# Kernel optimization log

Hardware: AMD Instinct MI355X
Metric: run time of the kernel (lower is better)

Reference implementation:

```python
import jax, jax.numpy as jnp
import numpy as np

EMB = 1024
HEADS = 16
SCALE = (EMB // HEADS) ** (-0.5)


def setup_inputs() -> dict:
    key = jax.random.key(0)
    k1, k2, k3, k4, k5 = jax.random.split(key, 5)
    x = jax.random.normal(k1, (2, 2048, EMB), dtype=jnp.float32)
    w_qkv = jax.random.normal(k2, (EMB, 3 * EMB), dtype=jnp.float32) * (EMB ** -0.5)
    b_qkv = jax.random.normal(k3, (3 * EMB,), dtype=jnp.float32) * 0.02
    w_proj = jax.random.normal(k4, (EMB, EMB), dtype=jnp.float32) * (EMB ** -0.5)
    b_proj = jax.random.normal(k5, (EMB,), dtype=jnp.float32) * 0.02
    return {"x": x, "w_qkv": w_qkv, "b_qkv": b_qkv, "w_proj": w_proj, "b_proj": b_proj}


def reference(x, w_qkv, b_qkv, w_proj, b_proj):
    b, n, d = x.shape
    # qkv projection; split last dim as (heads, head_dim, 3) exactly like the
    # torch reshape, then permute to (3, b, h, n, head_dim)
    qkv = (x @ w_qkv + b_qkv).reshape(b, n, HEADS, -1, 3)
    qkv = jnp.transpose(qkv, (4, 0, 2, 1, 3))
    q, k, v = qkv[0], qkv[1], qkv[2]
    energy = jnp.einsum('bhqd,bhkd->bhqk', q, k)  # full n x n scores
    att = jax.nn.softmax(energy, axis=-1) * SCALE  # softmax THEN scale (as in source)
    out = jnp.einsum('bhqk,bhkd->bhqd', att, v)
    out = jnp.transpose(out, (0, 2, 1, 3)).reshape(b, n, d)
    return out @ w_proj + b_proj
```

## Files before the change

kernel.cpp:

```cpp
#include <hip/hip_runtime.h>
#include <cstdint>

#define SEQ   2048
#define BATCH 2
#define EMB   1024
#define NH    16
#define HD    64
#define MROWS (BATCH*SEQ)
#define NQKV  (3*EMB)
#define SCALE 0.125f
#define L2E   1.4426950408889634f

typedef _Float16 half8 __attribute__((ext_vector_type(8)));
typedef _Float16 half4 __attribute__((ext_vector_type(4)));
typedef __fp16   fp16x2 __attribute__((ext_vector_type(2)));
typedef float    floatx4 __attribute__((ext_vector_type(4)));

#define MFMA(a,b,c) __builtin_amdgcn_mfma_f32_16x16x32_f16(a, b, c, 0, 0, 0)

__device__ __forceinline__ void async16(const void* g, const void* l) {
    __builtin_amdgcn_global_load_lds(
        (const __attribute__((address_space(1))) unsigned int*)(uintptr_t)g,
        (__attribute__((address_space(3))) unsigned int*)(uint32_t)(uintptr_t)l,
        16, 0, 0);
}

__global__ void k_split(const float* __restrict__ src, _Float16* __restrict__ hi, int n4) {
    int i = blockIdx.x * blockDim.x + threadIdx.x;
    if (i >= n4) return;
    float4 v = ((const float4*)src)[i];
    half4 h;
    h[0] = (_Float16)v.x;
    h[1] = (_Float16)v.y;
    h[2] = (_Float16)v.z;
    h[3] = (_Float16)v.w;
    ((half4*)hi)[i] = h;
}

__global__ void k_transpose_split(const float* __restrict__ w, _Float16* __restrict__ hi,
                                  int K, int N) {
    __shared__ float t[32][33];
    int n0 = blockIdx.x * 32, k0 = blockIdx.y * 32;
    int tx = threadIdx.x, ty = threadIdx.y;
    #pragma unroll
    for (int i = 0; i < 4; i++)
        t[ty + i * 8][tx] = w[(size_t)(k0 + ty + i * 8) * N + n0 + tx];
    __syncthreads();
    #pragma unroll
    for (int i = 0; i < 4; i++) {
        float v = t[tx][ty + i * 8];
        hi[(size_t)(n0 + ty + i * 8) * K + k0 + tx] = (_Float16)v;
    }
}

template<int MODE>
__global__ __launch_bounds__(256, 2)
void k_gemm(const _Float16* __restrict__ A, const _Float16* __restrict__ Bt,
            const float* __restrict__ bias,
            _Float16* __restrict__ outQ, _Float16* __restrict__ outK,
            _Float16* __restrict__ outV, float* __restrict__ outC,
            int Mdim, int Ndim, int Kdim) {
    __shared__ _Float16 smem[2 * 128 * 32];
    _Float16* As = smem;
    _Float16* Bs = smem + 4096;

    const int tid = threadIdx.x;
    const int lane = tid & 63, wid = tid >> 6;
    const int quad = lane >> 4, l16 = lane & 15;
    const int wm = (wid >> 1) * 64, wn = (wid & 1) * 64;
    const int m0 = blockIdx.y * 128, n0 = blockIdx.x * 128;

    floatx4 acc[4][4];
    #pragma unroll
    for (int i = 0; i < 4; i++)
        #pragma unroll
        for (int j = 0; j < 4; j++)
            acc[i][j] = (floatx4){0.f, 0.f, 0.f, 0.f};

    for (int k0 = 0; k0 < Kdim; k0 += 32) {
        __syncthreads();
        #pragma unroll
        for (int i = 0; i < 2; i++) {
            int c = i * 256 + tid;
            int row = c >> 2, slot = c & 3;
            int q = slot ^ ((row >> 1) & 3);
            async16(A  + (size_t)(m0 + row) * Kdim + k0 + q * 8, As + c * 8);
            async16(Bt + (size_t)(n0 + row) * Kdim + k0 + q * 8, Bs + c * 8);
        }
        __syncthreads();

        half8 af[4], bf[4];
        #pragma unroll
        for (int t = 0; t < 4; t++) {
            int rowA = wm + t * 16 + l16;
            af[t] = *(const half8*)(As + rowA * 32 + (quad ^ ((rowA >> 1) & 3)) * 8);
            int rowB = wn + t * 16 + l16;
            bf[t] = *(const half8*)(Bs + rowB * 32 + (quad ^ ((rowB >> 1) & 3)) * 8);
        }
        #pragma unroll
        for (int mt = 0; mt < 4; mt++)
            #pragma unroll
            for (int nt = 0; nt < 4; nt++)
                acc[mt][nt] = MFMA(af[mt], bf[nt], acc[mt][nt]);
    }

    #pragma unroll
    for (int mt = 0; mt < 4; mt++) {
        int rowg = m0 + wm + mt * 16 + quad * 4;
        #pragma unroll
        for (int nt = 0; nt < 4; nt++) {
            int colg = n0 + wn + nt * 16 + l16;
            float bv = bias[colg];
            if (MODE == 0) {
                int h = colg / 192, rem = colg % 192;
                int d = rem / 3, which = rem % 3;
                #pragma unroll
                for (int r = 0; r < 4; r++) {
                    int m = rowg + r;
                    int b = m >> 11, s = m & (SEQ - 1);
                    int bh = b * NH + h;
                    _Float16 hv = (_Float16)(acc[mt][nt][r] + bv);
                    if (which == 0)      outQ[((size_t)bh * SEQ + s) * HD + d] = hv;
                    else if (which == 1) outK[((size_t)bh * SEQ + s) * HD + d] = hv;
                    else                 outV[((size_t)bh * HD + d) * SEQ + s] = hv;
                }
            } else {
                #pragma unroll
                for (int r = 0; r < 4; r++)
                    outC[(size_t)(rowg + r) * Ndim + colg] = acc[mt][nt][r] + bv;
            }
        }
    }
}

__device__ __forceinline__ int swzK(int row) { return (row ^ (row >> 2)) & 7; }
__device__ __forceinline__ int swzV(int row) { return (row ^ (row >> 1)) & 7; }

__global__ __launch_bounds__(256, 2)
void k_attn(const _Float16* __restrict__ Q, const _Float16* __restrict__ K,
            const _Float16* __restrict__ Vt, _Float16* __restrict__ Aout) {
    __shared__ __align__(16) _Float16 Ks[128 * 64];
    __shared__ __align__(16) _Float16 Vs[64 * 128];

    const int tid = threadIdx.x;
    const int lane = tid & 63, wid = tid >> 6;
    const int quad = lane >> 4, l16 = lane & 15;

    const int n = blockIdx.x;
    const int bh = (n & 7) * 4 + (n >> 7);
    const int q0 = ((n >> 3) & 15) * 128;

    const _Float16* Qb = Q  + (size_t)bh * SEQ * HD;
    const _Float16* Kb = K  + (size_t)bh * SEQ * HD;
    const _Float16* Vb = Vt + (size_t)bh * HD * SEQ;

    const int rA = ((l16 >> 2) << 3) | (l16 & 3);
    const int grayl = (l16 ^ (l16 >> 1)) & 7;

    half8 qf[2][2];
    #pragma unroll
    for (int qt = 0; qt < 2; qt++)
        #pragma unroll
        for (int kc = 0; kc < 2; kc++)
            qf[qt][kc] = *(const half8*)(Qb + (size_t)(q0 + wid * 32 + qt * 16 + l16) * HD
                                          + kc * 32 + quad * 8);

    floatx4 o[2][4];
    float mi[2] = {-1e30f, -1e30f}, li[2] = {0.f, 0.f};
    #pragma unroll
    for (int qt = 0; qt < 2; qt++)
        #pragma unroll
        for (int dt = 0; dt < 4; dt++) o[qt][dt] = (floatx4){0.f, 0.f, 0.f, 0.f};

    for (int kv0 = 0; kv0 < SEQ; kv0 += 128) {
        __syncthreads();
        #pragma unroll
        for (int i = 0; i < 4; i++) {
            int c = i * 256 + tid;
            {
                int row = c >> 3, pos = c & 7;
                int q = pos ^ swzK(row);
                async16(Kb + (size_t)(kv0 + row) * HD + q * 8, Ks + c * 8);
            }
            {
                int row = c >> 4, pos = c & 15;
                int q = (pos & 8) | ((pos & 7) ^ swzV(row));
                async16(Vb + (size_t)row * SEQ + kv0 + q * 8, Vs + c * 8);
            }
        }
        __syncthreads();

        floatx4 sv[4][2][2];
        #pragma unroll
        for (int u = 0; u < 4; u++)
            #pragma unroll
            for (int e = 0; e < 2; e++) {
                int row = u * 32 + e * 4 + rA;
                int sw = swzK(row);
                const _Float16* base = Ks + row * 64;
                half8 kf0 = *(const half8*)(base + ((quad ^ sw) << 3));
                half8 kf1 = *(const half8*)(base + (((quad + 4) ^ sw) << 3));
                floatx4 z = (floatx4){0.f, 0.f, 0.f, 0.f};
                #pragma unroll
                for (int qt = 0; qt < 2; qt++) {
                    floatx4 s = MFMA(kf0, qf[qt][0], z);
                    sv[u][e][qt] = MFMA(kf1, qf[qt][1], s);
                }
            }

        #pragma unroll
        for (int qt = 0; qt < 2; qt++) {
            float mb = -1e30f;
            #pragma unroll
            for (int u = 0; u < 4; u++)
                #pragma unroll
                for (int e = 0; e < 2; e++)
                    #pragma unroll
                    for (int r = 0; r < 4; r++)
                        mb = fmaxf(mb, sv[u][e][qt][r]);
            mb = fmaxf(mb, __shfl_xor(mb, 16));
            mb = fmaxf(mb, __shfl_xor(mb, 32));
            float Mn = fmaxf(mi[qt], mb * L2E);
            float al = __builtin_amdgcn_exp2f(mi[qt] - Mn);
            mi[qt] = Mn;
            li[qt] *= al;
            float alq[4];
            #pragma unroll
            for (int r = 0; r < 4; r++)
                alq[r] = __shfl(al, quad * 4 + r);
            #pragma unroll
            for (int dt = 0; dt < 4; dt++)
                #pragma unroll
                for (int r = 0; r < 4; r++)
                    o[qt][dt][r] *= alq[r];
        }

        #pragma unroll
        for (int u = 0; u < 4; u++) {
            half8 af[2];
            #pragma unroll
            for (int qt = 0; qt < 2; qt++) {
                float p[8];
                float rs = 0.f;
                #pragma unroll
                for (int r = 0; r < 4; r++) {
                    p[r]     = __builtin_amdgcn_exp2f(fmaf(sv[u][0][qt][r], L2E, -mi[qt]));
                    p[4 + r] = __builtin_amdgcn_exp2f(fmaf(sv[u][1][qt][r], L2E, -mi[qt]));
                }
                #pragma unroll
                for (int r = 0; r < 8; r++) rs += p[r];
                li[qt] += rs;
                union { fp16x2 h2[4]; half8 v; } pk;
                pk.h2[0] = __builtin_amdgcn_cvt_pkrtz(p[0], p[1]);
                pk.h2[1] = __builtin_amdgcn_cvt_pkrtz(p[2], p[3]);
                pk.h2[2] = __builtin_amdgcn_cvt_pkrtz(p[4], p[5]);
                pk.h2[3] = __builtin_amdgcn_cvt_pkrtz(p[6], p[7]);
                af[qt] = pk.v;
            }
            int q = u * 4 + quad;
            int slotbase = (q & 8) | ((q & 7) ^ grayl);
            #pragma unroll
            for (int dt = 0; dt < 4; dt++) {
                int row = dt * 16 + l16;
                half8 vf = *(const half8*)(Vs + row * 128 + slotbase * 8);
                o[0][dt] = MFMA(af[0], vf, o[0][dt]);
                o[1][dt] = MFMA(af[1], vf, o[1][dt]);
            }
        }
    }

    float lv[2];
    #pragma unroll
    for (int qt = 0; qt < 2; qt++) {
        float l = li[qt];
        l += __shfl_xor(l, 16);
        l += __shfl_xor(l, 32);
        lv[qt] = l;
    }
    int b = bh >> 4, h = bh & 15;
    #pragma unroll
    for (int qt = 0; qt < 2; qt++)
        #pragma unroll
        for (int r = 0; r < 4; r++) {
            float l = __shfl(lv[qt], quad * 4 + r);
            float inv = SCALE / l;
            int srow = q0 + wid * 32 + qt * 16 + quad * 4 + r;
            #pragma unroll
            for (int dt = 0; dt < 4; dt++) {
                int col = h * HD + dt * 16 + l16;
                Aout[(size_t)(b * SEQ + srow) * EMB + col] = (_Float16)(o[qt][dt][r] * inv);
            }
        }
}

extern "C" void kernel_launch(void* const* d_in, const int* in_sizes, int n_in,
                              void* d_out, int out_size, void* d_ws, size_t ws_size,
                              hipStream_t stream) {
    (void)in_sizes; (void)n_in; (void)out_size; (void)ws_size;
    const float* x      = (const float*)d_in[0];
    const float* w_qkv  = (const float*)d_in[1];
    const float* b_qkv  = (const float*)d_in[2];
    const float* w_proj = (const float*)d_in[3];
    const float* b_proj = (const float*)d_in[4];

    char* ws = (char*)d_ws;
    const size_t MB = 1ull << 20;
    _Float16* x_hi  = (_Float16*)(ws + 0 * MB);
    _Float16* wq_hi = (_Float16*)(ws + 8 * MB);
    _Float16* wp_hi = (_Float16*)(ws + 14 * MB);
    _Float16* Qb    = (_Float16*)(ws + 16 * MB);
    _Float16* Kb    = (_Float16*)(ws + 24 * MB);
    _Float16* Vtb   = (_Float16*)(ws + 32 * MB);
    _Float16* attb  = (_Float16*)(ws + 40 * MB);

    k_split<<<(MROWS * EMB / 4) / 256, 256, 0, stream>>>(x, x_hi, MROWS * EMB / 4);
    k_transpose_split<<<dim3(NQKV / 32, EMB / 32), dim3(32, 8), 0, stream>>>(
        w_qkv, wq_hi, EMB, NQKV);
    k_transpose_split<<<dim3(EMB / 32, EMB / 32), dim3(32, 8), 0, stream>>>(
        w_proj, wp_hi, EMB, EMB);
    k_gemm<0><<<dim3(NQKV / 128, MROWS / 128), 256, 0, stream>>>(
        x_hi, wq_hi, b_qkv, Qb, Kb, Vtb, nullptr, MROWS, NQKV, EMB);
    k_attn<<<dim3(512), 256, 0, stream>>>(Qb, Kb, Vtb, attb);
    k_gemm<1><<<dim3(EMB / 128, MROWS / 128), 256, 0, stream>>>(
        attb, wp_hi, b_proj, nullptr, nullptr, nullptr,
        (float*)d_out, MROWS, EMB, EMB);
}
```

Baseline: 209.8 us.

## Double-buffer attention K/V loads, compute row sums via MFMA, narrow proj GEMM tile

```diff
diff --git a/kernel.cpp b/kernel.cpp
--- a/kernel.cpp
+++ b/kernel.cpp
@@ -53,28 +53,30 @@
     }
 }
 
-template<int MODE>
+template<int MODE, int NT>
 __global__ __launch_bounds__(256, 2)
 void k_gemm(const _Float16* __restrict__ A, const _Float16* __restrict__ Bt,
             const float* __restrict__ bias,
             _Float16* __restrict__ outQ, _Float16* __restrict__ outK,
             _Float16* __restrict__ outV, float* __restrict__ outC,
             int Mdim, int Ndim, int Kdim) {
-    __shared__ _Float16 smem[2 * 128 * 32];
+    constexpr int WN  = NT / 2;
+    constexpr int NTI = WN / 16;
+    __shared__ _Float16 smem[(128 + NT) * 32];
     _Float16* As = smem;
-    _Float16* Bs = smem + 4096;
+    _Float16* Bs = smem + 128 * 32;
 
     const int tid = threadIdx.x;
     const int lane = tid & 63, wid = tid >> 6;
     const int quad = lane >> 4, l16 = lane & 15;
-    const int wm = (wid >> 1) * 64, wn = (wid & 1) * 64;
-    const int m0 = blockIdx.y * 128, n0 = blockIdx.x * 128;
-
-    floatx4 acc[4][4];
+    const int wm = (wid >> 1) * 64, wn = (wid & 1) * WN;
+    const int m0 = blockIdx.y * 128, n0 = blockIdx.x * NT;
+
+    floatx4 acc[4][NTI];
     #pragma unroll
     for (int i = 0; i < 4; i++)
         #pragma unroll
-        for (int j = 0; j < 4; j++)
+        for (int j = 0; j < NTI; j++)
             acc[i][j] = (floatx4){0.f, 0.f, 0.f, 0.f};
 
     for (int k0 = 0; k0 < Kdim; k0 += 32) {
@@ -84,23 +86,32 @@
             int c = i * 256 + tid;
             int row = c >> 2, slot = c & 3;
             int q = slot ^ ((row >> 1) & 3);
-            async16(A  + (size_t)(m0 + row) * Kdim + k0 + q * 8, As + c * 8);
+            async16(A + (size_t)(m0 + row) * Kdim + k0 + q * 8, As + c * 8);
+        }
+        #pragma unroll
+        for (int i = 0; i < NT / 64; i++) {
+            int c = i * 256 + tid;
+            int row = c >> 2, slot = c & 3;
+            int q = slot ^ ((row >> 1) & 3);
             async16(Bt + (size_t)(n0 + row) * Kdim + k0 + q * 8, Bs + c * 8);
         }
         __syncthreads();
 
-        half8 af[4], bf[4];
+        half8 af[4], bf[NTI];
         #pragma unroll
         for (int t = 0; t < 4; t++) {
             int rowA = wm + t * 16 + l16;
             af[t] = *(const half8*)(As + rowA * 32 + (quad ^ ((rowA >> 1) & 3)) * 8);
+        }
+        #pragma unroll
+        for (int t = 0; t < NTI; t++) {
             int rowB = wn + t * 16 + l16;
             bf[t] = *(const half8*)(Bs + rowB * 32 + (quad ^ ((rowB >> 1) & 3)) * 8);
         }
         #pragma unroll
         for (int mt = 0; mt < 4; mt++)
             #pragma unroll
-            for (int nt = 0; nt < 4; nt++)
+            for (int nt = 0; nt < NTI; nt++)
                 acc[mt][nt] = MFMA(af[mt], bf[nt], acc[mt][nt]);
     }
 
@@ -108,7 +119,7 @@
     for (int mt = 0; mt < 4; mt++) {
         int rowg = m0 + wm + mt * 16 + quad * 4;
         #pragma unroll
-        for (int nt = 0; nt < 4; nt++) {
+        for (int nt = 0; nt < NTI; nt++) {
             int colg = n0 + wn + nt * 16 + l16;
             float bv = bias[colg];
             if (MODE == 0) {
@@ -139,8 +150,8 @@
 __global__ __launch_bounds__(256, 2)
 void k_attn(const _Float16* __restrict__ Q, const _Float16* __restrict__ K,
             const _Float16* __restrict__ Vt, _Float16* __restrict__ Aout) {
-    __shared__ __align__(16) _Float16 Ks[128 * 64];
-    __shared__ __align__(16) _Float16 Vs[64 * 128];
+    __shared__ __align__(16) _Float16 Ks[2][128 * 64];
+    __shared__ __align__(16) _Float16 Vs[2][80 * 128];
 
     const int tid = threadIdx.x;
     const int lane = tid & 63, wid = tid >> 6;
@@ -157,6 +168,15 @@
     const int rA = ((l16 >> 2) << 3) | (l16 & 3);
     const int grayl = (l16 ^ (l16 >> 1)) & 7;
 
+    {
+        half8 one8;
+        #pragma unroll
+        for (int r = 0; r < 8; r++) one8[r] = (_Float16)1.0f;
+        ((half8*)(Vs[0] + 64 * 128))[tid] = one8;
+        ((half8*)(Vs[1] + 64 * 128))[tid] = one8;
+    }
+    __syncthreads();
+
     half8 qf[2][2];
     #pragma unroll
     for (int qt = 0; qt < 2; qt++)
@@ -165,30 +185,44 @@
             qf[qt][kc] = *(const half8*)(Qb + (size_t)(q0 + wid * 32 + qt * 16 + l16) * HD
                                           + kc * 32 + quad * 8);
 
-    floatx4 o[2][4];
-    float mi[2] = {-1e30f, -1e30f}, li[2] = {0.f, 0.f};
-    #pragma unroll
-    for (int qt = 0; qt < 2; qt++)
+    #pragma unroll
+    for (int i = 0; i < 4; i++) {
+        int c = i * 256 + tid;
+        int rowK = c >> 3, posK = c & 7;
+        async16(Kb + (size_t)rowK * HD + (posK ^ swzK(rowK)) * 8, Ks[0] + c * 8);
+        int rowV = c >> 4, posV = c & 15;
+        int qv = (posV & 8) | ((posV & 7) ^ swzV(rowV));
+        async16(Vb + (size_t)rowV * SEQ + qv * 8, Vs[0] + c * 8);
+    }
+
+    floatx4 o[2][4], o_l[2];
+    float mi[2] = {-1e30f, -1e30f};
+    #pragma unroll
+    for (int qt = 0; qt < 2; qt++) {
         #pragma unroll
         for (int dt = 0; dt < 4; dt++) o[qt][dt] = (floatx4){0.f, 0.f, 0.f, 0.f};
-
-    for (int kv0 = 0; kv0 < SEQ; kv0 += 128) {
-        __syncthreads();
+        o_l[qt] = (floatx4){0.f, 0.f, 0.f, 0.f};
+    }
+
+    #pragma unroll 2
+    for (int t = 0; t < 16; t++) {
+        const int p = t & 1;
+        const int kvn = ((t + 1) & 15) * 128;
         #pragma unroll
         for (int i = 0; i < 4; i++) {
             int c = i * 256 + tid;
-            {
-                int row = c >> 3, pos = c & 7;
-                int q = pos ^ swzK(row);
-                async16(Kb + (size_t)(kv0 + row) * HD + q * 8, Ks + c * 8);
-            }
-            {
-                int row = c >> 4, pos = c & 15;
-                int q = (pos & 8) | ((pos & 7) ^ swzV(row));
-                async16(Vb + (size_t)row * SEQ + kv0 + q * 8, Vs + c * 8);
-            }
-        }
-        __syncthreads();
+            int rowK = c >> 3, posK = c & 7;
+            async16(Kb + (size_t)(kvn + rowK) * HD + (posK ^ swzK(rowK)) * 8,
+                    Ks[p ^ 1] + c * 8);
+            int rowV = c >> 4, posV = c & 15;
+            int qv = (posV & 8) | ((posV & 7) ^ swzV(rowV));
+            async16(Vb + (size_t)rowV * SEQ + kvn + qv * 8, Vs[p ^ 1] + c * 8);
+        }
+        asm volatile("s_waitcnt vmcnt(8)" ::: "memory");
+        asm volatile("s_barrier" ::: "memory");
+
+        const _Float16* Ksp = Ks[p];
+        const _Float16* Vsp = Vs[p];
 
         floatx4 sv[4][2][2];
         #pragma unroll
@@ -197,7 +231,7 @@
             for (int e = 0; e < 2; e++) {
                 int row = u * 32 + e * 4 + rA;
                 int sw = swzK(row);
-                const _Float16* base = Ks + row * 64;
+                const _Float16* base = Ksp + row * 64;
                 half8 kf0 = *(const half8*)(base + ((quad ^ sw) << 3));
                 half8 kf1 = *(const half8*)(base + (((quad + 4) ^ sw) << 3));
                 floatx4 z = (floatx4){0.f, 0.f, 0.f, 0.f};
@@ -223,7 +257,6 @@
             float Mn = fmaxf(mi[qt], mb * L2E);
             float al = __builtin_amdgcn_exp2f(mi[qt] - Mn);
             mi[qt] = Mn;
-            li[qt] *= al;
             float alq[4];
             #pragma unroll
             for (int r = 0; r < 4; r++)
@@ -233,6 +266,9 @@
                 #pragma unroll
                 for (int r = 0; r < 4; r++)
                     o[qt][dt][r] *= alq[r];
+            #pragma unroll
+            for (int r = 0; r < 4; r++)
+                o_l[qt][r] *= alq[r];
         }
 
         #pragma unroll
@@ -240,21 +276,17 @@
             half8 af[2];
             #pragma unroll
             for (int qt = 0; qt < 2; qt++) {
-                float p[8];
-                float rs = 0.f;
+                float p0[8];
                 #pragma unroll
                 for (int r = 0; r < 4; r++) {
-                    p[r]     = __builtin_amdgcn_exp2f(fmaf(sv[u][0][qt][r], L2E, -mi[qt]));
-                    p[4 + r] = __builtin_amdgcn_exp2f(fmaf(sv[u][1][qt][r], L2E, -mi[qt]));
+                    p0[r]     = __builtin_amdgcn_exp2f(fmaf(sv[u][0][qt][r], L2E, -mi[qt]));
+                    p0[4 + r] = __builtin_amdgcn_exp2f(fmaf(sv[u][1][qt][r], L2E, -mi[qt]));
                 }
-                #pragma unroll
-                for (int r = 0; r < 8; r++) rs += p[r];
-                li[qt] += rs;
                 union { fp16x2 h2[4]; half8 v; } pk;
-                pk.h2[0] = __builtin_amdgcn_cvt_pkrtz(p[0], p[1]);
-                pk.h2[1] = __builtin_amdgcn_cvt_pkrtz(p[2], p[3]);
-                pk.h2[2] = __builtin_amdgcn_cvt_pkrtz(p[4], p[5]);
-                pk.h2[3] = __builtin_amdgcn_cvt_pkrtz(p[6], p[7]);
+                pk.h2[0] = __builtin_amdgcn_cvt_pkrtz(p0[0], p0[1]);
+                pk.h2[1] = __builtin_amdgcn_cvt_pkrtz(p0[2], p0[3]);
+                pk.h2[2] = __builtin_amdgcn_cvt_pkrtz(p0[4], p0[5]);
+                pk.h2[3] = __builtin_amdgcn_cvt_pkrtz(p0[6], p0[7]);
                 af[qt] = pk.v;
             }
             int q = u * 4 + quad;
@@ -262,28 +294,24 @@
             #pragma unroll
             for (int dt = 0; dt < 4; dt++) {
                 int row = dt * 16 + l16;
-                half8 vf = *(const half8*)(Vs + row * 128 + slotbase * 8);
+                half8 vf = *(const half8*)(Vsp + row * 128 + slotbase * 8);
                 o[0][dt] = MFMA(af[0], vf, o[0][dt]);
                 o[1][dt] = MFMA(af[1], vf, o[1][dt]);
             }
-        }
-    }
-
-    float lv[2];
-    #pragma unroll
-    for (int qt = 0; qt < 2; qt++) {
-        float l = li[qt];
-        l += __shfl_xor(l, 16);
-        l += __shfl_xor(l, 32);
-        lv[qt] = l;
-    }
+            half8 vfl = *(const half8*)(Vsp + (64 + l16) * 128 + slotbase * 8);
+            o_l[0] = MFMA(af[0], vfl, o_l[0]);
+            o_l[1] = MFMA(af[1], vfl, o_l[1]);
+        }
+
+        asm volatile("s_barrier" ::: "memory");
+    }
+
     int b = bh >> 4, h = bh & 15;
     #pragma unroll
     for (int qt = 0; qt < 2; qt++)
         #pragma unroll
         for (int r = 0; r < 4; r++) {
-            float l = __shfl(lv[qt], quad * 4 + r);
-            float inv = SCALE / l;
+            float inv = SCALE / o_l[qt][r];
             int srow = q0 + wid * 32 + qt * 16 + quad * 4 + r;
             #pragma unroll
             for (int dt = 0; dt < 4; dt++) {
@@ -318,10 +346,10 @@
         w_qkv, wq_hi, EMB, NQKV);
     k_transpose_split<<<dim3(EMB / 32, EMB / 32), dim3(32, 8), 0, stream>>>(
         w_proj, wp_hi, EMB, EMB);
-    k_gemm<0><<<dim3(NQKV / 128, MROWS / 128), 256, 0, stream>>>(
+    k_gemm<0, 128><<<dim3(NQKV / 128, MROWS / 128), 256, 0, stream>>>(
         x_hi, wq_hi, b_qkv, Qb, Kb, Vtb, nullptr, MROWS, NQKV, EMB);
     k_attn<<<dim3(512), 256, 0, stream>>>(Qb, Kb, Vtb, attb);
-    k_gemm<1><<<dim3(EMB / 128, MROWS / 128), 256, 0, stream>>>(
+    k_gemm<1, 64><<<dim3(EMB / 64, MROWS / 128), 256, 0, stream>>>(
         attb, wp_hi, b_proj, nullptr, nullptr, nullptr,
         (float*)d_out, MROWS, EMB, EMB);
 }
```

After: 197.7 us. -5.8%, faster.
